# Optimization experiments

Measured on AMD Instinct MI355X. Metric: run time of the kernel, lower is better.

## Reference

```python
import jax, jax.numpy as jnp
import numpy as np

B, T, C, H = 2, 2048, 1024, 16
HD = C // H  # head_dim = 64


def setup_inputs() -> dict:
    key = jax.random.key(0)
    k1, k2, k3 = jax.random.split(key, 3)
    x = jax.random.normal(k1, (B, T, C), dtype=jnp.float32)
    w_attn = jax.random.normal(k2, (3 * C, C), dtype=jnp.float32) * 0.02
    w_proj = jax.random.normal(k3, (C, C), dtype=jnp.float32) * 0.02
    # RoPE frequencies: theta_i = 10000^(-2i/head_dim)
    inv_freq = 1.0 / (10000.0 ** (jnp.arange(0, HD, 2, dtype=jnp.float32) / HD))  # (HD//2,)
    angles = jnp.arange(T, dtype=jnp.float32)[:, None] * inv_freq[None, :]        # (T, HD//2)
    return {
        "x": x,
        "w_attn": w_attn,
        "w_proj": w_proj,
        "freqs_cos": jnp.cos(angles),
        "freqs_sin": jnp.sin(angles),
    }


def _rope(t, cos, sin):
    # t: (B, T, H, HD); cos/sin: (T, HD//2) broadcast to (1, T, 1, HD//2)
    te = t[..., 0::2]
    to = t[..., 1::2]
    c = cos[None, :, None, :]
    s = sin[None, :, None, :]
    re = te * c - to * s
    ro = te * s + to * c
    # interleave back: (..., HD//2, 2) -> (..., HD)
    return jnp.stack([re, ro], axis=-1).reshape(t.shape)


def reference(x, w_attn, w_proj, freqs_cos, freqs_sin):
    b, t, c = x.shape
    qkv = jnp.einsum('btc,fc->btf', x, w_attn)          # (B, T, 3C)
    q, k, v = jnp.split(qkv, 3, axis=2)
    q = q.reshape(b, t, H, HD)
    k = k.reshape(b, t, H, HD)
    v = v.reshape(b, t, H, HD)
    q = _rope(q, freqs_cos, freqs_sin)
    k = _rope(k, freqs_cos, freqs_sin)
    # causal SDPA
    scale = 1.0 / np.sqrt(HD).astype(np.float32)
    scores = jnp.einsum('bqhd,bkhd->bhqk', q, k) * scale  # (B, H, T, T)
    mask = jnp.tril(jnp.ones((t, t), dtype=bool))
    scores = jnp.where(mask[None, None, :, :], scores, jnp.finfo(scores.dtype).min)
    attn = jax.nn.softmax(scores, axis=-1)
    y = jnp.einsum('bhqk,bkhd->bqhd', attn, v).reshape(b, t, c)
    return jnp.einsum('btc,oc->bto', y, w_proj)
```

## Files before the change

### kernel.cpp

```cpp
#include <hip/hip_runtime.h>
#include <math.h>

#define B_  2
#define T_  2048
#define C_  1024
#define H_  16
#define HD_ 64
#define F3_ 3072

typedef __attribute__((ext_vector_type(8))) __bf16 bf16x8;
typedef __attribute__((ext_vector_type(4))) float  f32x4;

__device__ __forceinline__ ushort f2bf(float f) {
  uint32_t u = __builtin_bit_cast(uint32_t, f);
  u += 0x7fff + ((u >> 16) & 1);
  return (ushort)(u >> 16);
}
__device__ __forceinline__ float bf2f(ushort u) {
  return __builtin_bit_cast(float, (uint32_t)u << 16);
}
__device__ __forceinline__ void gll16(void* lds, const void* g) {
  __builtin_amdgcn_global_load_lds(
      (const __attribute__((address_space(1))) void*)g,
      (__attribute__((address_space(3))) void*)lds, 16, 0, 0);
}

__global__ __launch_bounds__(256) void cvt_f32_bf16(const float* __restrict__ in,
                                                    ushort* __restrict__ out, int n4) {
  int i = blockIdx.x * 256 + threadIdx.x;
  if (i >= n4) return;
  float4 v = ((const float4*)in)[i];
  ushort4 o;
  o.x = f2bf(v.x); o.y = f2bf(v.y); o.z = f2bf(v.z); o.w = f2bf(v.w);
  ((ushort4*)out)[i] = o;
}

template<int MODE>
__global__ __launch_bounds__(256) void gemm_mfma(
    const ushort* __restrict__ A, const ushort* __restrict__ Bm,
    void* __restrict__ Cout, ushort* __restrict__ vT,
    int M, int N, int K)
{
  __shared__ ushort As[128][64];
  __shared__ ushort Bs[128][64];
  const int tid  = threadIdx.x;
  const int lane = tid & 63, w = tid >> 6;
  const int wr = w >> 1, wc = w & 1;
  const int ll = lane & 15, lg = lane >> 4;
  const int r8 = lane >> 3;
  const int gc = ((lane & 7) ^ r8) << 3;
  const int m0 = blockIdx.x * 128, n0 = blockIdx.y * 128;

  f32x4 acc[4][4] = {};

  for (int k0 = 0; k0 < K; k0 += 64) {
    __syncthreads();
#pragma unroll
    for (int iss = 0; iss < 4; ++iss) {
      int rb = w * 32 + iss * 8;
      gll16(&As[rb][0], A  + (size_t)(m0 + rb + r8) * K + k0 + gc);
      gll16(&Bs[rb][0], Bm + (size_t)(n0 + rb + r8) * K + k0 + gc);
    }
    __syncthreads();
#pragma unroll
    for (int ks = 0; ks < 2; ++ks) {
      const int sw = ((ks * 4 + lg) ^ (ll & 7)) * 8;
      bf16x8 af[4], bfr[4];
#pragma unroll
      for (int mi = 0; mi < 4; ++mi)
        af[mi] = *(const bf16x8*)&As[wr * 64 + mi * 16 + ll][sw];
#pragma unroll
      for (int ni = 0; ni < 4; ++ni)
        bfr[ni] = *(const bf16x8*)&Bs[wc * 64 + ni * 16 + ll][sw];
#pragma unroll
      for (int mi = 0; mi < 4; ++mi)
#pragma unroll
        for (int ni = 0; ni < 4; ++ni)
          acc[mi][ni] = __builtin_amdgcn_mfma_f32_16x16x32_bf16(
              af[mi], bfr[ni], acc[mi][ni], 0, 0, 0);
    }
  }

  const int mrow = wr * 64 + lg * 4;
  const int ncol = wc * 64 + ll;
  if (MODE == 0) {
    float* C = (float*)Cout;
#pragma unroll
    for (int mi = 0; mi < 4; ++mi)
#pragma unroll
      for (int ni = 0; ni < 4; ++ni)
#pragma unroll
        for (int r = 0; r < 4; ++r)
          C[(size_t)(m0 + mrow + mi * 16 + r) * N + n0 + ncol + ni * 16] =
              acc[mi][ni][r];
  } else {
    if (n0 < 2 * C_) {
      ushort* q = (ushort*)Cout;
#pragma unroll
      for (int mi = 0; mi < 4; ++mi)
#pragma unroll
        for (int ni = 0; ni < 4; ++ni)
#pragma unroll
          for (int r = 0; r < 4; ++r)
            q[(size_t)(m0 + mrow + mi * 16 + r) * F3_ + n0 + ncol + ni * 16] =
                f2bf(acc[mi][ni][r]);
    } else {
      const int bb = m0 >> 11;
      const int tb = (m0 & 2047) + mrow;
#pragma unroll
      for (int mi = 0; mi < 4; ++mi)
#pragma unroll
        for (int ni = 0; ni < 4; ++ni) {
          int f  = n0 + ncol + ni * 16 - 2 * C_;
          int hh = f >> 6, d = f & 63;
          ushort4 o;
          o.x = f2bf(acc[mi][ni][0]); o.y = f2bf(acc[mi][ni][1]);
          o.z = f2bf(acc[mi][ni][2]); o.w = f2bf(acc[mi][ni][3]);
          *(ushort4*)&vT[(((size_t)(bb * H_ + hh) * HD_ + d) << 11) + tb + mi * 16] = o;
        }
    }
  }
}

__global__ __launch_bounds__(256) void rope_bf(ushort* __restrict__ qkv,
                                               const float* __restrict__ fcos,
                                               const float* __restrict__ fsin) {
  int idx = blockIdx.x * 256 + threadIdx.x;
  int i2 = idx & 15;
  int h  = (idx >> 4) & 15;
  int t  = (idx >> 8) & 2047;
  int b  = idx >> 19;
  int fi = t * 32 + i2 * 2;
  float c0 = fcos[fi], s0 = fsin[fi], c1 = fcos[fi + 1], s1 = fsin[fi + 1];
  size_t base = (size_t)(b * T_ + t) * F3_ + h * HD_ + i2 * 4;
  ushort4 qv = *(ushort4*)&qkv[base];
  ushort4 qo;
  { float e = bf2f(qv.x), o = bf2f(qv.y);
    qo.x = f2bf((e * c0 - o * s0) * 0.125f);
    qo.y = f2bf((e * s0 + o * c0) * 0.125f); }
  { float e = bf2f(qv.z), o = bf2f(qv.w);
    qo.z = f2bf((e * c1 - o * s1) * 0.125f);
    qo.w = f2bf((e * s1 + o * c1) * 0.125f); }
  *(ushort4*)&qkv[base] = qo;
  ushort4 kv = *(ushort4*)&qkv[base + C_];
  ushort4 ko;
  { float e = bf2f(kv.x), o = bf2f(kv.y);
    ko.x = f2bf(e * c0 - o * s0);
    ko.y = f2bf(e * s0 + o * c0); }
  { float e = bf2f(kv.z), o = bf2f(kv.w);
    ko.z = f2bf(e * c1 - o * s1);
    ko.w = f2bf(e * s1 + o * c1); }
  *(ushort4*)&qkv[base + C_] = ko;
}

__global__ __launch_bounds__(256) void attn_mfma(
    const ushort* __restrict__ qkv, const ushort* __restrict__ vT,
    ushort* __restrict__ y)
{
  __shared__ ushort Qs[64][64];
  __shared__ ushort Ks[2][64][64], VTs[2][64][64];
  __shared__ ushort Ps[4][16][72];

  const int qt = 31 - blockIdx.y;
  const int bh = blockIdx.x;
  const int b = bh >> 4, h = bh & 15;
  const int q0 = qt * 64;
  const int tid = threadIdx.x, lane = tid & 63, w = tid >> 6;
  const int ll = lane & 15, lg = lane >> 4;
  const int r8 = lane >> 3;
  const int gc = ((lane & 7) ^ r8) << 3;
  const float NEG = -3.0e38f;

  const ushort* qb = qkv + (size_t)(b * T_) * F3_ + h * HD_;
  const ushort* kb = qb + C_;
  const ushort* vb = vT + ((size_t)(b * H_ + h) * HD_ << 11);

#pragma unroll
  for (int iss = 0; iss < 2; ++iss) {
    int rb = w * 16 + iss * 8;
    gll16(&Qs[rb][0], qb + (size_t)(q0 + rb + r8) * F3_ + gc);
    gll16(&Ks[0][rb][0],  kb + (size_t)(rb + r8) * F3_ + gc);
    gll16(&VTs[0][rb][0], vb + ((size_t)(rb + r8) << 11) + gc);
  }
  __syncthreads();

  bf16x8 qf[2];
#pragma unroll
  for (int ks = 0; ks < 2; ++ks)
    qf[ks] = *(const bf16x8*)&Qs[w * 16 + ll][((ks * 4 + lg) ^ (ll & 7)) * 8];

  f32x4 oacc[4] = {};
  float m_ = NEG, l_ = 0.f;
  int cur = 0;

  for (int kt = 0; kt <= qt; ++kt) {
    if (kt < qt) {
#pragma unroll
      for (int iss = 0; iss < 2; ++iss) {
        int rb = w * 16 + iss * 8;
        gll16(&Ks[cur ^ 1][rb][0],
              kb + (size_t)((kt + 1) * 64 + rb + r8) * F3_ + gc);
        gll16(&VTs[cur ^ 1][rb][0],
              vb + ((size_t)(rb + r8) << 11) + (kt + 1) * 64 + gc);
      }
    }

    f32x4 sacc[4] = {};
#pragma unroll
    for (int ks = 0; ks < 2; ++ks) {
      const int sw = ((ks * 4 + lg) ^ (ll & 7)) * 8;
      bf16x8 kf[4];
#pragma unroll
      for (int j = 0; j < 4; ++j)
        kf[j] = *(const bf16x8*)&Ks[cur][j * 16 + ll][sw];
#pragma unroll
      for (int j = 0; j < 4; ++j)
        sacc[j] = __builtin_amdgcn_mfma_f32_16x16x32_bf16(kf[j], qf[ks], sacc[j], 0, 0, 0);
    }

    if (kt == qt) {
#pragma unroll
      for (int j = 0; j < 4; ++j)
#pragma unroll
        for (int r = 0; r < 4; ++r)
          if (j * 16 + lg * 4 + r > w * 16 + ll) sacc[j][r] = NEG;
    }

    float tmax;
    {
      float t0 = fmaxf(fmaxf(sacc[0][0], sacc[0][1]), fmaxf(sacc[0][2], sacc[0][3]));
      float t1 = fmaxf(fmaxf(sacc[1][0], sacc[1][1]), fmaxf(sacc[1][2], sacc[1][3]));
      float t2 = fmaxf(fmaxf(sacc[2][0], sacc[2][1]), fmaxf(sacc[2][2], sacc[2][3]));
      float t3 = fmaxf(fmaxf(sacc[3][0], sacc[3][1]), fmaxf(sacc[3][2], sacc[3][3]));
      tmax = fmaxf(fmaxf(t0, t1), fmaxf(t2, t3));
      tmax = fmaxf(tmax, __shfl_xor(tmax, 16));
      tmax = fmaxf(tmax, __shfl_xor(tmax, 32));
    }
    if (!__all(tmax <= m_ + 8.f)) {
      float mnew = fmaxf(m_, tmax);
      float al = __expf(m_ - mnew);
      l_ *= al;
      m_ = mnew;
#pragma unroll
      for (int r = 0; r < 4; ++r) {
        float alr = __shfl(al, lg * 4 + r);
#pragma unroll
        for (int dj = 0; dj < 4; ++dj) oacc[dj][r] *= alr;
      }
    }
    float psum = 0.f;
#pragma unroll
    for (int j = 0; j < 4; ++j) {
      float p0 = __expf(sacc[j][0] - m_);
      float p1 = __expf(sacc[j][1] - m_);
      float p2 = __expf(sacc[j][2] - m_);
      float p3 = __expf(sacc[j][3] - m_);
      psum += (p0 + p1) + (p2 + p3);
      ushort4 pk;
      pk.x = f2bf(p0); pk.y = f2bf(p1); pk.z = f2bf(p2); pk.w = f2bf(p3);
      *(ushort4*)&Ps[w][ll][j * 16 + lg * 4] = pk;
    }
    psum += __shfl_xor(psum, 16);
    psum += __shfl_xor(psum, 32);
    l_ += psum;

#pragma unroll
    for (int ks = 0; ks < 2; ++ks) {
      bf16x8 pf = *(const bf16x8*)&Ps[w][ll][ks * 32 + lg * 8];
      const int sw = ((ks * 4 + lg) ^ (ll & 7)) * 8;
#pragma unroll
      for (int dj = 0; dj < 4; ++dj) {
        bf16x8 vf = *(const bf16x8*)&VTs[cur][dj * 16 + ll][sw];
        oacc[dj] = __builtin_amdgcn_mfma_f32_16x16x32_bf16(pf, vf, oacc[dj], 0, 0, 0);
      }
    }

    __syncthreads();
    cur ^= 1;
  }

#pragma unroll
  for (int r = 0; r < 4; ++r) {
    float lr = __shfl(l_, lg * 4 + r);
    float inv = 1.0f / lr;
    int row = q0 + w * 16 + lg * 4 + r;
#pragma unroll
    for (int dj = 0; dj < 4; ++dj)
      y[(size_t)(b * T_ + row) * C_ + h * HD_ + dj * 16 + ll] =
          f2bf(oacc[dj][r] * inv);
  }
}

extern "C" void kernel_launch(void* const* d_in, const int* in_sizes, int n_in,
                              void* d_out, int out_size, void* d_ws, size_t ws_size,
                              hipStream_t stream) {
  const float* x      = (const float*)d_in[0];
  const float* w_attn = (const float*)d_in[1];
  const float* w_proj = (const float*)d_in[2];
  const float* fcos   = (const float*)d_in[3];
  const float* fsin   = (const float*)d_in[4];
  float* out = (float*)d_out;

  ushort* xb   = (ushort*)d_ws;
  ushort* wab  = xb   + (size_t)4096 * 1024;
  ushort* wpb  = wab  + (size_t)3072 * 1024;
  ushort* qkvb = wpb  + (size_t)1024 * 1024;
  ushort* vt   = qkvb + (size_t)4096 * 3072;
  ushort* yb   = vt   + (size_t)32 * 64 * 2048;

  cvt_f32_bf16<<<4096, 256, 0, stream>>>(x,      xb,  1048576);
  cvt_f32_bf16<<<3072, 256, 0, stream>>>(w_attn, wab,  786432);
  cvt_f32_bf16<<<1024, 256, 0, stream>>>(w_proj, wpb,  262144);

  { dim3 g(32, 24); gemm_mfma<1><<<g, 256, 0, stream>>>(xb, wab, qkvb, vt, 4096, F3_, C_); }
  rope_bf<<<4096, 256, 0, stream>>>(qkvb, fcos, fsin);
  { dim3 g(32, 32); attn_mfma<<<g, 256, 0, stream>>>(qkvb, vt, yb); }
  { dim3 g(32, 8);  gemm_mfma<0><<<g, 256, 0, stream>>>(yb, wpb, out, nullptr, 4096, C_, C_); }
}
```

Measured before the change: 115.0 us.

## Use 128-row query tiles with 8 waves sharing K/V loads, exp2 softmax

The attention kernel now processes 128 query rows per block with 512 threads (8 waves), so each K/V tile loaded into LDS is shared by twice as many waves and global K/V traffic is halved. The block order is changed to interleave heavy and light causal tiles, and waves whose rows lie entirely before a K tile skip that tile. The query scale is folded with log2(e) so softmax uses exp2f. P is converted to bf16 by truncation instead of rounding, and Q shares LDS with P to save space. Risks include idle waves on the diagonal tiles, a lower block count for scheduling, and slightly less accurate P values.

```diff
diff --git a/kernel.cpp b/kernel.cpp
--- a/kernel.cpp
+++ b/kernel.cpp
@@ -122,6 +122,7 @@
   }
 }
 
+#define QSC 0.18033688f
 __global__ __launch_bounds__(256) void rope_bf(ushort* __restrict__ qkv,
                                                const float* __restrict__ fcos,
                                                const float* __restrict__ fsin) {
@@ -136,11 +137,11 @@
   ushort4 qv = *(ushort4*)&qkv[base];
   ushort4 qo;
   { float e = bf2f(qv.x), o = bf2f(qv.y);
-    qo.x = f2bf((e * c0 - o * s0) * 0.125f);
-    qo.y = f2bf((e * s0 + o * c0) * 0.125f); }
+    qo.x = f2bf((e * c0 - o * s0) * QSC);
+    qo.y = f2bf((e * s0 + o * c0) * QSC); }
   { float e = bf2f(qv.z), o = bf2f(qv.w);
-    qo.z = f2bf((e * c1 - o * s1) * 0.125f);
-    qo.w = f2bf((e * s1 + o * c1) * 0.125f); }
+    qo.z = f2bf((e * c1 - o * s1) * QSC);
+    qo.w = f2bf((e * s1 + o * c1) * QSC); }
   *(ushort4*)&qkv[base] = qo;
   ushort4 kv = *(ushort4*)&qkv[base + C_];
   ushort4 ko;
@@ -153,18 +154,20 @@
   *(ushort4*)&qkv[base + C_] = ko;
 }
 
-__global__ __launch_bounds__(256) void attn_mfma(
+__global__ __launch_bounds__(512) void attn_mfma(
     const ushort* __restrict__ qkv, const ushort* __restrict__ vT,
     ushort* __restrict__ y)
 {
-  __shared__ ushort Qs[64][64];
-  __shared__ ushort Ks[2][64][64], VTs[2][64][64];
-  __shared__ ushort Ps[4][16][72];
-
-  const int qt = 31 - blockIdx.y;
+  __shared__ __align__(16) ushort PsQ[8][16][72];
+  __shared__ __align__(16) ushort Ks[2][64][64], VTs[2][64][64];
+  ushort (*Qs)[64] = (ushort (*)[64])&PsQ[0][0][0];
+
+  const int by = blockIdx.y;
+  const int qy = (by < 8) ? 15 - by : by - 8;
   const int bh = blockIdx.x;
   const int b = bh >> 4, h = bh & 15;
-  const int q0 = qt * 64;
+  const int q0 = qy * 128;
+  const int nkt = 2 * qy + 2;
   const int tid = threadIdx.x, lane = tid & 63, w = tid >> 6;
   const int ll = lane & 15, lg = lane >> 4;
   const int r8 = lane >> 3;
@@ -179,6 +182,9 @@
   for (int iss = 0; iss < 2; ++iss) {
     int rb = w * 16 + iss * 8;
     gll16(&Qs[rb][0], qb + (size_t)(q0 + rb + r8) * F3_ + gc);
+  }
+  {
+    int rb = w * 8;
     gll16(&Ks[0][rb][0],  kb + (size_t)(rb + r8) * F3_ + gc);
     gll16(&VTs[0][rb][0], vb + ((size_t)(rb + r8) << 11) + gc);
   }
@@ -188,90 +194,94 @@
 #pragma unroll
   for (int ks = 0; ks < 2; ++ks)
     qf[ks] = *(const bf16x8*)&Qs[w * 16 + ll][((ks * 4 + lg) ^ (ll & 7)) * 8];
+  __syncthreads();
 
   f32x4 oacc[4] = {};
   float m_ = NEG, l_ = 0.f;
   int cur = 0;
 
-  for (int kt = 0; kt <= qt; ++kt) {
-    if (kt < qt) {
-#pragma unroll
-      for (int iss = 0; iss < 2; ++iss) {
-        int rb = w * 16 + iss * 8;
-        gll16(&Ks[cur ^ 1][rb][0],
-              kb + (size_t)((kt + 1) * 64 + rb + r8) * F3_ + gc);
-        gll16(&VTs[cur ^ 1][rb][0],
-              vb + ((size_t)(rb + r8) << 11) + (kt + 1) * 64 + gc);
-      }
-    }
-
-    f32x4 sacc[4] = {};
-#pragma unroll
-    for (int ks = 0; ks < 2; ++ks) {
-      const int sw = ((ks * 4 + lg) ^ (ll & 7)) * 8;
-      bf16x8 kf[4];
-#pragma unroll
-      for (int j = 0; j < 4; ++j)
-        kf[j] = *(const bf16x8*)&Ks[cur][j * 16 + ll][sw];
-#pragma unroll
-      for (int j = 0; j < 4; ++j)
-        sacc[j] = __builtin_amdgcn_mfma_f32_16x16x32_bf16(kf[j], qf[ks], sacc[j], 0, 0, 0);
-    }
-
-    if (kt == qt) {
-#pragma unroll
-      for (int j = 0; j < 4; ++j)
-#pragma unroll
-        for (int r = 0; r < 4; ++r)
-          if (j * 16 + lg * 4 + r > w * 16 + ll) sacc[j][r] = NEG;
-    }
-
-    float tmax;
-    {
-      float t0 = fmaxf(fmaxf(sacc[0][0], sacc[0][1]), fmaxf(sacc[0][2], sacc[0][3]));
-      float t1 = fmaxf(fmaxf(sacc[1][0], sacc[1][1]), fmaxf(sacc[1][2], sacc[1][3]));
-      float t2 = fmaxf(fmaxf(sacc[2][0], sacc[2][1]), fmaxf(sacc[2][2], sacc[2][3]));
-      float t3 = fmaxf(fmaxf(sacc[3][0], sacc[3][1]), fmaxf(sacc[3][2], sacc[3][3]));
-      tmax = fmaxf(fmaxf(t0, t1), fmaxf(t2, t3));
-      tmax = fmaxf(tmax, __shfl_xor(tmax, 16));
-      tmax = fmaxf(tmax, __shfl_xor(tmax, 32));
-    }
-    if (!__all(tmax <= m_ + 8.f)) {
-      float mnew = fmaxf(m_, tmax);
-      float al = __expf(m_ - mnew);
-      l_ *= al;
-      m_ = mnew;
-#pragma unroll
-      for (int r = 0; r < 4; ++r) {
-        float alr = __shfl(al, lg * 4 + r);
-#pragma unroll
-        for (int dj = 0; dj < 4; ++dj) oacc[dj][r] *= alr;
-      }
-    }
-    float psum = 0.f;
-#pragma unroll
-    for (int j = 0; j < 4; ++j) {
-      float p0 = __expf(sacc[j][0] - m_);
-      float p1 = __expf(sacc[j][1] - m_);
-      float p2 = __expf(sacc[j][2] - m_);
-      float p3 = __expf(sacc[j][3] - m_);
-      psum += (p0 + p1) + (p2 + p3);
-      ushort4 pk;
-      pk.x = f2bf(p0); pk.y = f2bf(p1); pk.z = f2bf(p2); pk.w = f2bf(p3);
-      *(ushort4*)&Ps[w][ll][j * 16 + lg * 4] = pk;
-    }
-    psum += __shfl_xor(psum, 16);
-    psum += __shfl_xor(psum, 32);
-    l_ += psum;
-
-#pragma unroll
-    for (int ks = 0; ks < 2; ++ks) {
-      bf16x8 pf = *(const bf16x8*)&Ps[w][ll][ks * 32 + lg * 8];
-      const int sw = ((ks * 4 + lg) ^ (ll & 7)) * 8;
-#pragma unroll
-      for (int dj = 0; dj < 4; ++dj) {
-        bf16x8 vf = *(const bf16x8*)&VTs[cur][dj * 16 + ll][sw];
-        oacc[dj] = __builtin_amdgcn_mfma_f32_16x16x32_bf16(pf, vf, oacc[dj], 0, 0, 0);
+  for (int kt = 0; kt < nkt; ++kt) {
+    if (kt + 1 < nkt) {
+      int rb = w * 8;
+      gll16(&Ks[cur ^ 1][rb][0],
+            kb + (size_t)((kt + 1) * 64 + rb + r8) * F3_ + gc);
+      gll16(&VTs[cur ^ 1][rb][0],
+            vb + ((size_t)(rb + r8) << 11) + (kt + 1) * 64 + gc);
+    }
+
+    if (kt * 64 <= q0 + w * 16 + 15) {
+      f32x4 sacc[4] = {};
+#pragma unroll
+      for (int ks = 0; ks < 2; ++ks) {
+        const int sw = ((ks * 4 + lg) ^ (ll & 7)) * 8;
+        bf16x8 kf[4];
+#pragma unroll
+        for (int j = 0; j < 4; ++j)
+          kf[j] = *(const bf16x8*)&Ks[cur][j * 16 + ll][sw];
+#pragma unroll
+        for (int j = 0; j < 4; ++j)
+          sacc[j] = __builtin_amdgcn_mfma_f32_16x16x32_bf16(kf[j], qf[ks], sacc[j], 0, 0, 0);
+      }
+
+      if (kt * 64 + 63 > q0 + w * 16) {
+        int rowg = q0 + w * 16 + ll;
+#pragma unroll
+        for (int j = 0; j < 4; ++j)
+#pragma unroll
+          for (int r = 0; r < 4; ++r)
+            if (kt * 64 + j * 16 + lg * 4 + r > rowg) sacc[j][r] = NEG;
+      }
+
+      float tmax;
+      {
+        float t0 = fmaxf(fmaxf(sacc[0][0], sacc[0][1]), fmaxf(sacc[0][2], sacc[0][3]));
+        float t1 = fmaxf(fmaxf(sacc[1][0], sacc[1][1]), fmaxf(sacc[1][2], sacc[1][3]));
+        float t2 = fmaxf(fmaxf(sacc[2][0], sacc[2][1]), fmaxf(sacc[2][2], sacc[2][3]));
+        float t3 = fmaxf(fmaxf(sacc[3][0], sacc[3][1]), fmaxf(sacc[3][2], sacc[3][3]));
+        tmax = fmaxf(fmaxf(t0, t1), fmaxf(t2, t3));
+        tmax = fmaxf(tmax, __shfl_xor(tmax, 16));
+        tmax = fmaxf(tmax, __shfl_xor(tmax, 32));
+      }
+      if (!__all(tmax <= m_ + 11.5441f)) {
+        float mnew = fmaxf(m_, tmax);
+        float al = exp2f(m_ - mnew);
+        l_ *= al;
+        m_ = mnew;
+#pragma unroll
+        for (int r = 0; r < 4; ++r) {
+          float alr = __shfl(al, lg * 4 + r);
+#pragma unroll
+          for (int dj = 0; dj < 4; ++dj) oacc[dj][r] *= alr;
+        }
+      }
+      float psum = 0.f;
+#pragma unroll
+      for (int j = 0; j < 4; ++j) {
+        float p0 = exp2f(sacc[j][0] - m_);
+        float p1 = exp2f(sacc[j][1] - m_);
+        float p2 = exp2f(sacc[j][2] - m_);
+        float p3 = exp2f(sacc[j][3] - m_);
+        psum += (p0 + p1) + (p2 + p3);
+        uint u0 = __builtin_bit_cast(uint32_t, p0) >> 16;
+        uint u1 = __builtin_bit_cast(uint32_t, p1) & 0xffff0000u;
+        uint u2 = __builtin_bit_cast(uint32_t, p2) >> 16;
+        uint u3 = __builtin_bit_cast(uint32_t, p3) & 0xffff0000u;
+        uint2 pk = make_uint2(u0 | u1, u2 | u3);
+        *(uint2*)&PsQ[w][ll][j * 16 + lg * 4] = pk;
+      }
+      psum += __shfl_xor(psum, 16);
+      psum += __shfl_xor(psum, 32);
+      l_ += psum;
+
+#pragma unroll
+      for (int ks = 0; ks < 2; ++ks) {
+        bf16x8 pf = *(const bf16x8*)&PsQ[w][ll][ks * 32 + lg * 8];
+        const int sw = ((ks * 4 + lg) ^ (ll & 7)) * 8;
+#pragma unroll
+        for (int dj = 0; dj < 4; ++dj) {
+          bf16x8 vf = *(const bf16x8*)&VTs[cur][dj * 16 + ll][sw];
+          oacc[dj] = __builtin_amdgcn_mfma_f32_16x16x32_bf16(pf, vf, oacc[dj], 0, 0, 0);
+        }
       }
     }
 
@@ -314,6 +324,6 @@
 
   { dim3 g(32, 24); gemm_mfma<1><<<g, 256, 0, stream>>>(xb, wab, qkvb, vt, 4096, F3_, C_); }
   rope_bf<<<4096, 256, 0, stream>>>(qkvb, fcos, fsin);
-  { dim3 g(32, 32); attn_mfma<<<g, 256, 0, stream>>>(qkvb, vt, yb); }
+  { dim3 g(32, 16); attn_mfma<<<g, 512, 0, stream>>>(qkvb, vt, yb); }
   { dim3 g(32, 8);  gemm_mfma<0><<<g, 256, 0, stream>>>(yb, wpb, out, nullptr, 4096, C_, C_); }
 }
```

New measurement: 126.8 us. +10.2%, slower.
